# Kernel optimization log

Hardware: AMD Instinct MI355X
Metric: run time of the kernel (lower is better)

Reference implementation:

```python
import jax, jax.numpy as jnp
import numpy as np

B, S, D, H = 4, 2048, 512, 8
INNER = D  # assumed AttentionHead.inner_size == size (naive single-head attention)


def setup_inputs() -> dict:
    key = jax.random.key(0)
    ks = jax.random.split(key, 8)
    scale = 0.02
    return {
        "emb_input": jax.random.normal(ks[0], (B, S, D), dtype=jnp.float32),
        "Wq": jax.random.normal(ks[1], (H, D, INNER), dtype=jnp.float32) * scale,
        "bq": jnp.zeros((H, INNER), dtype=jnp.float32),
        "Wk": jax.random.normal(ks[2], (H, D, INNER), dtype=jnp.float32) * scale,
        "bk": jnp.zeros((H, INNER), dtype=jnp.float32),
        "Wv": jax.random.normal(ks[3], (H, D, INNER), dtype=jnp.float32) * scale,
        "bv": jnp.zeros((H, INNER), dtype=jnp.float32),
        "Wp": jax.random.normal(ks[4], (H * INNER, D), dtype=jnp.float32) * scale,
        "bp": jnp.zeros((D,), dtype=jnp.float32),
    }


def reference(emb_input, Wq, bq, Wk, bk, Wv, bv, Wp, bp):
    # All heads batched into one einsum instead of a Python loop over submodules.
    x = emb_input  # [B, S, D]
    q = jnp.einsum("bsd,hde->bhse", x, Wq) + bq[None, :, None, :]  # [B,H,S,E]
    k = jnp.einsum("bsd,hde->bhse", x, Wk) + bk[None, :, None, :]
    v = jnp.einsum("bsd,hde->bhse", x, Wv) + bv[None, :, None, :]
    scores = jnp.einsum("bhse,bhte->bhst", q, k) / jnp.sqrt(
        jnp.asarray(INNER, dtype=x.dtype)
    )  # [B,H,S,S]
    attn = jax.nn.softmax(scores, axis=-1)
    o = jnp.einsum("bhst,bhte->bhse", attn, v)  # [B,H,S,E]
    # concat over heads (dim=2 in torch => feature dim after per-head outputs)
    o = jnp.transpose(o, (0, 2, 1, 3)).reshape(B, S, H * INNER)
    return o @ Wp + bp  # [B, S, D]
```

## Files before the change

kernel.cpp:

```cpp
#include <hip/hip_runtime.h>


typedef short s8v __attribute__((ext_vector_type(8)));
typedef float f4v __attribute__((ext_vector_type(4)));
typedef unsigned short us;
typedef us us4v __attribute__((ext_vector_type(4)));
typedef us us8v __attribute__((ext_vector_type(8)));

__device__ inline us f2b(float f) {
  union { float f; unsigned u; } v; v.f = f;
  unsigned r = v.u + 0x7FFFu + ((v.u >> 16) & 1u);
  return (us)(r >> 16);
}
__device__ inline float b2f(us b) {
  union { unsigned u; float f; } v; v.u = ((unsigned)b) << 16;
  return v.f;
}

__device__ inline void gld16(const us* g, us* l) {
  __builtin_amdgcn_global_load_lds(
      (const __attribute__((address_space(1))) void*)g,
      (__attribute__((address_space(3))) void*)l, 16, 0, 0);
}

template <int EPI>
__global__ __launch_bounds__(256, 4) void gemm_nt(
    const us* __restrict__ A, int lda, long long sA0, long long sA1,
    const us* __restrict__ Bm, int ldb, long long sB0, long long sB1,
    const float* __restrict__ bias, long long sbias,
    void* __restrict__ Cv, int ldc, long long sC0, long long sC1,
    int K, float alpha, int L) {
  __shared__ us As[2][4096];
  __shared__ us Bs[2][4096];
  const int t = threadIdx.x;
  const int wv = t >> 6, ln = t & 63;
  const int m16 = ln & 15, quad = ln >> 4;

  const int gx = gridDim.x, gxy = gx * gridDim.y;
  const int nblk = gxy * gridDim.z;
  const int flat = blockIdx.x + gx * blockIdx.y + gxy * blockIdx.z;
  const int per = nblk >> 3;
  const int nid = (flat & 7) * per + (flat >> 3);
  const int bz = nid / gxy, rem = nid % gxy;
  const int by = rem / gx, bx = rem % gx;

  const long long row0 = (long long)by * 128;
  const long long col0 = (long long)bx * 128;
  const int zo = bz >> L, zi = bz & ((1 << L) - 1);
  const us* Az = A + zo * sA0 + zi * sA1;
  const us* Bz = Bm + zo * sB0 + zi * sB1;

  int offA[2], offB[2];
#pragma unroll
  for (int j = 0; j < 2; ++j) {
    const int c = t + 256 * j;
    const int mb = c >> 6, qd = (c >> 4) & 3, mm = c & 15;
    offA[j] = (int)((row0 + mb * 16 + mm) * (long long)lda + qd * 8);
    offB[j] = (int)((col0 + mb * 16 + mm) * (long long)ldb + qd * 8);
  }

  f4v acc[4][4];
#pragma unroll
  for (int r = 0; r < 4; ++r)
#pragma unroll
    for (int c = 0; c < 4; ++c) acc[r][c] = (f4v){0.f, 0.f, 0.f, 0.f};

  const int nk = K >> 5;
  const int fo = quad * 16 + m16;

#pragma unroll
  for (int j = 0; j < 2; ++j) {
    gld16(Az + offA[j], (us*)As[0] + (256 * j + wv * 64) * 8);
    gld16(Bz + offB[j], (us*)Bs[0] + (256 * j + wv * 64) * 8);
  }

  for (int i = 0; i < nk; ++i) {
    __syncthreads();
    const int cur = i & 1;
    if (i + 1 < nk) {
      const int kof = (i + 1) << 5;
#pragma unroll
      for (int j = 0; j < 2; ++j) {
        gld16(Az + offA[j] + kof, (us*)As[cur ^ 1] + (256 * j + wv * 64) * 8);
        gld16(Bz + offB[j] + kof, (us*)Bs[cur ^ 1] + (256 * j + wv * 64) * 8);
      }
    }
    s8v af[4], bf[4];
#pragma unroll
    for (int r = 0; r < 4; ++r)
      af[r] = *(const s8v*)&As[cur][(((wv & 1) * 4 + r) * 64 + fo) * 8];
#pragma unroll
    for (int c = 0; c < 4; ++c)
      bf[c] = *(const s8v*)&Bs[cur][(((wv >> 1) * 4 + c) * 64 + fo) * 8];
#pragma unroll
    for (int r = 0; r < 4; ++r)
#pragma unroll
      for (int c = 0; c < 4; ++c)
        acc[r][c] = __builtin_amdgcn_mfma_f32_16x16x32_bf16(af[r], bf[c], acc[r][c], 0, 0, 0);
  }

  const float* bz_ = bias ? (bias + zi * sbias) : (const float*)0;
#pragma unroll
  for (int r = 0; r < 4; ++r) {
    const long long gr0 = row0 + (wv & 1) * 64 + r * 16 + quad * 4;
#pragma unroll
    for (int c = 0; c < 4; ++c) {
      const long long gc = col0 + (wv >> 1) * 64 + c * 16 + m16;
      if (EPI == 1) {
        us* C = (us*)Cv + zo * sC0 + zi * sC1;
        const float bb = bz_ ? bz_[gc] : 0.f;
#pragma unroll
        for (int g = 0; g < 4; ++g)
          C[(gr0 + g) * (long long)ldc + gc] = f2b(acc[r][c][g] * alpha + bb);
      } else if (EPI == 2) {
        us* C = (us*)Cv + zo * sC0 + zi * sC1;
        const float bb = bz_ ? bz_[gc] : 0.f;
        us4v pk;
#pragma unroll
        for (int g = 0; g < 4; ++g) pk[g] = f2b(acc[r][c][g] * alpha + bb);
        *(us4v*)&C[gc * (long long)ldc + gr0] = pk;
      } else {
        float* C = (float*)Cv + zo * sC0 + zi * sC1;
        float* p = C + gr0 * ldc + gc;
#pragma unroll
        for (int g = 0; g < 4; ++g) p[(long long)g * ldc] += acc[r][c][g] * alpha;
      }
    }
  }
}

__global__ __launch_bounds__(256) void softmax_bf16(us* __restrict__ sc) {
  const int w = threadIdx.x >> 6, ln = threadIdx.x & 63;
  us* p = sc + ((long long)blockIdx.y * 2048 + (long long)(blockIdx.x * 4 + w)) * 2048;
  us8v raw[4];
  float vals[32];
#pragma unroll
  for (int j = 0; j < 4; ++j) raw[j] = *(const us8v*)(p + j * 512 + ln * 8);
  float m = -1e30f;
#pragma unroll
  for (int j = 0; j < 4; ++j)
#pragma unroll
    for (int u = 0; u < 8; ++u) {
      vals[j * 8 + u] = b2f(raw[j][u]);
      m = fmaxf(m, vals[j * 8 + u]);
    }
#pragma unroll
  for (int off = 32; off; off >>= 1) m = fmaxf(m, __shfl_xor(m, off, 64));
  float s = 0.f;
#pragma unroll
  for (int u = 0; u < 32; ++u) {
    vals[u] = __expf(vals[u] - m);
    s += vals[u];
  }
#pragma unroll
  for (int off = 32; off; off >>= 1) s += __shfl_xor(s, off, 64);
  const float inv = 1.f / s;
#pragma unroll
  for (int j = 0; j < 4; ++j) {
    us8v o;
#pragma unroll
    for (int u = 0; u < 8; ++u) o[u] = f2b(vals[j * 8 + u] * inv);
    *(us8v*)(p + j * 512 + ln * 8) = o;
  }
}

__global__ __launch_bounds__(256) void conv_bf16(const float* __restrict__ in,
                                                 us* __restrict__ out, int n4) {
  const int i = blockIdx.x * 256 + threadIdx.x;
  if (i < n4) {
    const float4 f = ((const float4*)in)[i];
    us4v o;
    o[0] = f2b(f.x); o[1] = f2b(f.y); o[2] = f2b(f.z); o[3] = f2b(f.w);
    ((us4v*)out)[i] = o;
  }
}

__global__ __launch_bounds__(256) void conv_transpose(const float* __restrict__ in,
                                                      us* __restrict__ out,
                                                      int R, int C) {
  __shared__ float tile[32][33];
  const int tx = threadIdx.x & 31, ty = threadIdx.x >> 5;
  const long long zo = (long long)blockIdx.z * R * C;
  const int r0 = blockIdx.y * 32, c0 = blockIdx.x * 32;
#pragma unroll
  for (int j = 0; j < 4; ++j)
    tile[ty + 8 * j][tx] = in[zo + (long long)(r0 + ty + 8 * j) * C + c0 + tx];
  __syncthreads();
#pragma unroll
  for (int j = 0; j < 4; ++j)
    out[zo + (long long)(c0 + ty + 8 * j) * R + r0 + tx] = f2b(tile[tx][ty + 8 * j]);
}

__global__ __launch_bounds__(256) void init_out_kernel(float* __restrict__ out,
                                                       const float* __restrict__ bp,
                                                       int total) {
  const int i = blockIdx.x * 256 + threadIdx.x;
  if (i < total) out[i] = bp[i & 511];
}

extern "C" void kernel_launch(void* const* d_in, const int* in_sizes, int n_in,
                              void* d_out, int out_size, void* d_ws, size_t ws_size,
                              hipStream_t stream) {
  constexpr int Bb = 4, S = 2048, D = 512, H = 8, E = 512, HE = 4096;
  const float* x  = (const float*)d_in[0];
  const float* Wq = (const float*)d_in[1];
  const float* bq = (const float*)d_in[2];
  const float* Wk = (const float*)d_in[3];
  const float* bk = (const float*)d_in[4];
  const float* Wv = (const float*)d_in[5];
  const float* bv = (const float*)d_in[6];
  const float* Wp = (const float*)d_in[7];
  const float* bp = (const float*)d_in[8];
  float* out = (float*)d_out;

  const long long SE = (long long)S * E, SS = (long long)S * S;
  const long long SD = (long long)S * D, ED = (long long)E * D;

  us* xh  = (us*)d_ws;
  us* WqT = xh + 4194304;
  us* WkT = WqT + 2097152;
  us* WvT = WkT + 2097152;
  us* WpT = WvT + 2097152;
  us* dyn = WpT + 2097152;

  const size_t fixedB = (size_t)(4194304 + 4 * 2097152) * 2;
  int HC = 8;
  while (HC > 1) {
    const size_t need = fixedB + (size_t)HC * (3 * (size_t)Bb * SE + (size_t)Bb * SS) * 2;
    if (need <= ws_size) break;
    HC >>= 1;
  }
  const int L = (HC == 8) ? 3 : (HC == 4) ? 2 : (HC == 2) ? 1 : 0;
  const int BHC = Bb * HC;

  us* qh = dyn;
  us* kh = qh + (size_t)BHC * SE;
  us* vT = kh + (size_t)BHC * SE;
  us* sc = vT + (size_t)BHC * SE;
  us* oh = qh;

  const dim3 tb(256);
  init_out_kernel<<<dim3((Bb * S * D + 255) / 256), tb, 0, stream>>>(out, bp, Bb * S * D);
  conv_bf16<<<dim3(4194304 / 4 / 256), tb, 0, stream>>>(x, xh, 4194304 / 4);
  conv_transpose<<<dim3(E / 32, D / 32, H), tb, 0, stream>>>(Wq, WqT, D, E);
  conv_transpose<<<dim3(E / 32, D / 32, H), tb, 0, stream>>>(Wk, WkT, D, E);
  conv_transpose<<<dim3(E / 32, D / 32, H), tb, 0, stream>>>(Wv, WvT, D, E);
  conv_transpose<<<dim3(D / 32, HE / 32, 1), tb, 0, stream>>>(Wp, WpT, HE, D);

  const float aS = 0.044194173824159216f;
  const dim3 gP(4, 16, BHC), gS(16, 16, BHC);

  for (int h0 = 0; h0 < H; h0 += HC) {
    gemm_nt<1><<<gP, tb, 0, stream>>>(
        xh, D, SD, 0, WqT + (long long)h0 * ED, D, 0, ED, bq + h0 * E, E,
        qh, E, (long long)HC * SE, SE, D, 1.f, L);
    gemm_nt<1><<<gP, tb, 0, stream>>>(
        xh, D, SD, 0, WkT + (long long)h0 * ED, D, 0, ED, bk + h0 * E, E,
        kh, E, (long long)HC * SE, SE, D, 1.f, L);
    gemm_nt<2><<<gP, tb, 0, stream>>>(
        xh, D, SD, 0, WvT + (long long)h0 * ED, D, 0, ED, bv + h0 * E, E,
        vT, S, (long long)HC * E * S, (long long)E * S, D, 1.f, L);
    gemm_nt<1><<<gS, tb, 0, stream>>>(
        qh, E, (long long)HC * SE, SE, kh, E, (long long)HC * SE, SE, nullptr, 0,
        sc, S, (long long)HC * SS, SS, E, aS, L);
    softmax_bf16<<<dim3(S / 4, BHC), tb, 0, stream>>>(sc);
    gemm_nt<1><<<gP, tb, 0, stream>>>(
        sc, S, (long long)HC * SS, SS, vT, S, (long long)HC * E * S, (long long)E * S,
        nullptr, 0, oh, HC * E, (long long)S * HC * E, E, S, 1.f, L);
    gemm_nt<4><<<dim3(4, 16, Bb), tb, 0, stream>>>(
        oh, HC * E, (long long)S * HC * E, 0, WpT + (long long)h0 * E, HE, 0, 0,
        nullptr, 0, out, D, SD, 0, HC * E, 1.f, 0);
  }
}
```

Before: 1.126 ms.

## Fuse Q/K/V projections into one GEMM and split output projection per head with atomics

Packs the transposed Wq/Wk/Wv per head chunk into one contiguous weight block, so a single GEMM launch computes Q, K and V and routes each column tile to its destination buffer (V stored transposed). The output projection is now split over heads as well, with one block per batch and head, and accumulates into the output with float atomicAdd. Both changes aim to launch more blocks and fewer kernels, improving GPU fill. The cost is atomic contention on the output across the eight heads and a nondeterministic summation order.

```diff
diff --git a/kernel.cpp b/kernel.cpp
--- a/kernel.cpp
+++ b/kernel.cpp
@@ -27,9 +27,11 @@
 __global__ __launch_bounds__(256, 4) void gemm_nt(
     const us* __restrict__ A, int lda, long long sA0, long long sA1,
     const us* __restrict__ Bm, int ldb, long long sB0, long long sB1,
-    const float* __restrict__ bias, long long sbias,
-    void* __restrict__ Cv, int ldc, long long sC0, long long sC1,
-    int K, float alpha, int L) {
+    const float* __restrict__ bias, const float* __restrict__ bias2,
+    const float* __restrict__ bias3,
+    void* __restrict__ Cv, void* __restrict__ C2, void* __restrict__ C3,
+    int ldc, long long sC0, long long sC1,
+    int K, float alpha, int L, int sbits) {
   __shared__ us As[2][4096];
   __shared__ us Bs[2][4096];
   const int t = threadIdx.x;
@@ -39,8 +41,8 @@
   const int gx = gridDim.x, gxy = gx * gridDim.y;
   const int nblk = gxy * gridDim.z;
   const int flat = blockIdx.x + gx * blockIdx.y + gxy * blockIdx.z;
-  const int per = nblk >> 3;
-  const int nid = (flat & 7) * per + (flat >> 3);
+  int nid = flat;
+  if ((nblk & 7) == 0) nid = (flat & 7) * (nblk >> 3) + (flat >> 3);
   const int bz = nid / gxy, rem = nid % gxy;
   const int by = rem / gx, bx = rem % gx;
 
@@ -99,7 +101,6 @@
         acc[r][c] = __builtin_amdgcn_mfma_f32_16x16x32_bf16(af[r], bf[c], acc[r][c], 0, 0, 0);
   }
 
-  const float* bz_ = bias ? (bias + zi * sbias) : (const float*)0;
 #pragma unroll
   for (int r = 0; r < 4; ++r) {
     const long long gr0 = row0 + (wv & 1) * 64 + r * 16 + quad * 4;
@@ -108,22 +109,42 @@
       const long long gc = col0 + (wv >> 1) * 64 + c * 16 + m16;
       if (EPI == 1) {
         us* C = (us*)Cv + zo * sC0 + zi * sC1;
-        const float bb = bz_ ? bz_[gc] : 0.f;
+        const float bb = bias ? bias[gc] : 0.f;
 #pragma unroll
         for (int g = 0; g < 4; ++g)
           C[(gr0 + g) * (long long)ldc + gc] = f2b(acc[r][c][g] * alpha + bb);
-      } else if (EPI == 2) {
-        us* C = (us*)Cv + zo * sC0 + zi * sC1;
-        const float bb = bz_ ? bz_[gc] : 0.f;
-        us4v pk;
-#pragma unroll
-        for (int g = 0; g < 4; ++g) pk[g] = f2b(acc[r][c][g] * alpha + bb);
-        *(us4v*)&C[gc * (long long)ldc + gr0] = pk;
+      } else if (EPI == 3) {
+        const int which = (int)(col0 >> sbits);
+        const int gsec = (int)gc & ((1 << sbits) - 1);
+        const int hc = gsec >> 9, e = (int)gc & 511;
+        const long long slice =
+            ((long long)zo * (1 << (sbits - 9)) + hc) * 1048576LL;
+        if (which == 0) {
+          us* C = (us*)Cv;
+          const float bb = bias[gsec];
+#pragma unroll
+          for (int g = 0; g < 4; ++g)
+            C[slice + (gr0 + g) * 512 + e] = f2b(acc[r][c][g] + bb);
+        } else if (which == 1) {
+          us* C = (us*)C2;
+          const float bb = bias2[gsec];
+#pragma unroll
+          for (int g = 0; g < 4; ++g)
+            C[slice + (gr0 + g) * 512 + e] = f2b(acc[r][c][g] + bb);
+        } else {
+          us* C = (us*)C3;
+          const float bb = bias3[gsec];
+          us4v pk;
+#pragma unroll
+          for (int g = 0; g < 4; ++g) pk[g] = f2b(acc[r][c][g] + bb);
+          *(us4v*)&C[slice + (long long)e * 2048 + gr0] = pk;
+        }
       } else {
-        float* C = (float*)Cv + zo * sC0 + zi * sC1;
+        float* C = (float*)Cv + zo * sC0;
         float* p = C + gr0 * ldc + gc;
 #pragma unroll
-        for (int g = 0; g < 4; ++g) p[(long long)g * ldc] += acc[r][c][g] * alpha;
+        for (int g = 0; g < 4; ++g)
+          atomicAdd(&p[(long long)g * ldc], acc[r][c][g] * alpha);
       }
     }
   }
@@ -177,18 +198,21 @@
 
 __global__ __launch_bounds__(256) void conv_transpose(const float* __restrict__ in,
                                                       us* __restrict__ out,
-                                                      int R, int C) {
+                                                      int R, int C, int Lc,
+                                                      int mask, long long sChunk) {
   __shared__ float tile[32][33];
   const int tx = threadIdx.x & 31, ty = threadIdx.x >> 5;
-  const long long zo = (long long)blockIdx.z * R * C;
+  const int z = blockIdx.z;
+  const long long zi = (long long)z * R * C;
+  us* dst = out + (long long)(z >> Lc) * sChunk + (long long)(z & mask) * R * C;
   const int r0 = blockIdx.y * 32, c0 = blockIdx.x * 32;
 #pragma unroll
   for (int j = 0; j < 4; ++j)
-    tile[ty + 8 * j][tx] = in[zo + (long long)(r0 + ty + 8 * j) * C + c0 + tx];
+    tile[ty + 8 * j][tx] = in[zi + (long long)(r0 + ty + 8 * j) * C + c0 + tx];
   __syncthreads();
 #pragma unroll
   for (int j = 0; j < 4; ++j)
-    out[zo + (long long)(c0 + ty + 8 * j) * R + r0 + tx] = f2b(tile[tx][ty + 8 * j]);
+    dst[(long long)(c0 + ty + 8 * j) * R + r0 + tx] = f2b(tile[tx][ty + 8 * j]);
 }
 
 __global__ __launch_bounds__(256) void init_out_kernel(float* __restrict__ out,
@@ -217,21 +241,20 @@
   const long long SD = (long long)S * D, ED = (long long)E * D;
 
   us* xh  = (us*)d_ws;
-  us* WqT = xh + 4194304;
-  us* WkT = WqT + 2097152;
-  us* WvT = WkT + 2097152;
-  us* WpT = WvT + 2097152;
+  us* W3  = xh + 4194304;
+  us* WpT = W3 + 6291456;
   us* dyn = WpT + 2097152;
 
-  const size_t fixedB = (size_t)(4194304 + 4 * 2097152) * 2;
+  const size_t fixedB = (size_t)(4194304 + 6291456 + 2097152) * 2;
   int HC = 8;
   while (HC > 1) {
     const size_t need = fixedB + (size_t)HC * (3 * (size_t)Bb * SE + (size_t)Bb * SS) * 2;
     if (need <= ws_size) break;
     HC >>= 1;
   }
-  const int L = (HC == 8) ? 3 : (HC == 4) ? 2 : (HC == 2) ? 1 : 0;
+  const int Lh = (HC == 8) ? 3 : (HC == 4) ? 2 : (HC == 2) ? 1 : 0;
   const int BHC = Bb * HC;
+  const int sbits = 9 + Lh;
 
   us* qh = dyn;
   us* kh = qh + (size_t)BHC * SE;
@@ -242,33 +265,37 @@
   const dim3 tb(256);
   init_out_kernel<<<dim3((Bb * S * D + 255) / 256), tb, 0, stream>>>(out, bp, Bb * S * D);
   conv_bf16<<<dim3(4194304 / 4 / 256), tb, 0, stream>>>(x, xh, 4194304 / 4);
-  conv_transpose<<<dim3(E / 32, D / 32, H), tb, 0, stream>>>(Wq, WqT, D, E);
-  conv_transpose<<<dim3(E / 32, D / 32, H), tb, 0, stream>>>(Wk, WkT, D, E);
-  conv_transpose<<<dim3(E / 32, D / 32, H), tb, 0, stream>>>(Wv, WvT, D, E);
-  conv_transpose<<<dim3(D / 32, HE / 32, 1), tb, 0, stream>>>(Wp, WpT, HE, D);
+  const long long sChunk = 3LL * HC * ED;
+  conv_transpose<<<dim3(16, 16, H), tb, 0, stream>>>(Wq, W3, D, E, Lh, HC - 1, sChunk);
+  conv_transpose<<<dim3(16, 16, H), tb, 0, stream>>>(Wk, W3 + HC * ED, D, E, Lh, HC - 1, sChunk);
+  conv_transpose<<<dim3(16, 16, H), tb, 0, stream>>>(Wv, W3 + 2 * HC * ED, D, E, Lh, HC - 1, sChunk);
+  conv_transpose<<<dim3(16, 128, 1), tb, 0, stream>>>(Wp, WpT, HE, D, 0, 0, 0);
 
   const float aS = 0.044194173824159216f;
-  const dim3 gP(4, 16, BHC), gS(16, 16, BHC);
-
-  for (int h0 = 0; h0 < H; h0 += HC) {
-    gemm_nt<1><<<gP, tb, 0, stream>>>(
-        xh, D, SD, 0, WqT + (long long)h0 * ED, D, 0, ED, bq + h0 * E, E,
-        qh, E, (long long)HC * SE, SE, D, 1.f, L);
-    gemm_nt<1><<<gP, tb, 0, stream>>>(
-        xh, D, SD, 0, WkT + (long long)h0 * ED, D, 0, ED, bk + h0 * E, E,
-        kh, E, (long long)HC * SE, SE, D, 1.f, L);
-    gemm_nt<2><<<gP, tb, 0, stream>>>(
-        xh, D, SD, 0, WvT + (long long)h0 * ED, D, 0, ED, bv + h0 * E, E,
-        vT, S, (long long)HC * E * S, (long long)E * S, D, 1.f, L);
+  const dim3 gQKV(3 * HC * E / 128, 16, Bb);
+  const dim3 gS(16, 16, BHC);
+  const dim3 gPV(4, 16, BHC);
+  const dim3 gOP(4, 16, BHC);
+
+  for (int c = 0; c < H / HC; ++c) {
+    const int h0 = c * HC;
+    gemm_nt<3><<<gQKV, tb, 0, stream>>>(
+        xh, D, SD, 0, W3 + c * sChunk, D, 0, 0,
+        bq + h0 * E, bk + h0 * E, bv + h0 * E,
+        qh, kh, vT, 512, 0, SE, D, 1.f, 0, sbits);
     gemm_nt<1><<<gS, tb, 0, stream>>>(
-        qh, E, (long long)HC * SE, SE, kh, E, (long long)HC * SE, SE, nullptr, 0,
-        sc, S, (long long)HC * SS, SS, E, aS, L);
+        qh, E, (long long)HC * SE, SE, kh, E, (long long)HC * SE, SE,
+        nullptr, nullptr, nullptr, sc, nullptr, nullptr,
+        S, (long long)HC * SS, SS, E, aS, Lh, 0);
     softmax_bf16<<<dim3(S / 4, BHC), tb, 0, stream>>>(sc);
-    gemm_nt<1><<<gP, tb, 0, stream>>>(
-        sc, S, (long long)HC * SS, SS, vT, S, (long long)HC * E * S, (long long)E * S,
-        nullptr, 0, oh, HC * E, (long long)S * HC * E, E, S, 1.f, L);
-    gemm_nt<4><<<dim3(4, 16, Bb), tb, 0, stream>>>(
-        oh, HC * E, (long long)S * HC * E, 0, WpT + (long long)h0 * E, HE, 0, 0,
-        nullptr, 0, out, D, SD, 0, HC * E, 1.f, 0);
-  }
-}
+    gemm_nt<1><<<gPV, tb, 0, stream>>>(
+        sc, S, (long long)HC * SS, SS, vT, S, (long long)HC * SE, SE,
+        nullptr, nullptr, nullptr, oh, nullptr, nullptr,
+        HC * E, (long long)S * HC * E, E, S, 1.f, Lh, 0);
+    gemm_nt<5><<<gOP, tb, 0, stream>>>(
+        oh, HC * E, (long long)S * HC * E, 512,
+        WpT + (long long)h0 * E, HE, 0, 512,
+        nullptr, nullptr, nullptr, out, nullptr, nullptr,
+        D, SD, 0, 512, 1.f, Lh, 0);
+  }
+}
```

Measured after the change: 1.104 ms. No clear change (-1.9%).
